# Performance work log

Measured on AMD Instinct MI355X. Metric: run time of the kernel, lower is better.

Reference implementation:

```python
import jax, jax.numpy as jnp
import numpy as np
import math

B, S, D, H, HD, R, F = 2, 2048, 1024, 16, 64, 32, 4096
EPS = 1e-5

def _layernorm(x, g, b):
    mu = jnp.mean(x, axis=-1, keepdims=True)
    var = jnp.mean(jnp.square(x - mu), axis=-1, keepdims=True)
    return (x - mu) * jax.lax.rsqrt(var + EPS) * g + b

def _gelu(x):
    # faithful tanh-approximation from the module
    c = math.sqrt(2.0 / math.pi)
    return 0.5 * x * (1.0 + jnp.tanh(c * (x + 0.044715 * x ** 3)))

def setup_inputs() -> dict:
    key = jax.random.key(0)
    ks = jax.random.split(key, 8)
    s = 0.02
    return dict(
        x=jax.random.normal(ks[0], (B, S, D), jnp.float32),
        ln1_g=jnp.ones((D,), jnp.float32), ln1_b=jnp.zeros((D,), jnp.float32),
        Wq=jax.random.normal(ks[1], (H, D, HD), jnp.float32) * s,
        bq=jnp.zeros((H, HD), jnp.float32),
        Wk=jax.random.normal(ks[2], (H, D, HD), jnp.float32) * s,
        bk=jnp.zeros((H, HD), jnp.float32),
        Wvd=jax.random.normal(ks[3], (H, D, R), jnp.float32) * s,
        bvd=jnp.zeros((H, R), jnp.float32),
        Wvu=jax.random.normal(ks[4], (H, R, HD), jnp.float32) * s,
        bvu=jnp.zeros((H, HD), jnp.float32),
        ln2_g=jnp.ones((D,), jnp.float32), ln2_b=jnp.zeros((D,), jnp.float32),
        W1=jax.random.normal(ks[5], (D, F), jnp.float32) * s,
        b1=jnp.zeros((F,), jnp.float32),
        W2=jax.random.normal(ks[6], (F, D), jnp.float32) * s,
        b2=jnp.zeros((D,), jnp.float32),
    )

def reference(x, ln1_g, ln1_b, Wq, bq, Wk, bk, Wvd, bvd, Wvu, bvu,
              ln2_g, ln2_b, W1, b1, W2, b2):
    Bx, Sx, Dx = x.shape
    y = x
    h = _layernorm(x, ln1_g, ln1_b)
    # all heads batched: [B,H,S,HD]
    q = jnp.einsum('bsd,hde->bhse', h, Wq) + bq[None, :, None, :]
    k = jnp.einsum('bsd,hde->bhse', h, Wk) + bk[None, :, None, :]
    vd = jnp.einsum('bsd,hdr->bhsr', h, Wvd) + bvd[None, :, None, :]
    v = jnp.einsum('bhsr,hre->bhse', vd, Wvu) + bvu[None, :, None, :]
    scores = jnp.einsum('bhse,bhte->bhst', q, k) / math.sqrt(Dx)  # NB: scaled by embed dim, as in source
    i = jnp.arange(Sx)
    mask = i[None, :] < i[:, None]  # key index < query index is masked (reversed causal, faithful)
    scores = jnp.where(mask[None, None, :, :], -jnp.inf, scores)
    attn = jax.nn.softmax(scores, axis=-1)
    o = jnp.einsum('bhst,bhte->bhse', attn, v)
    o = o.transpose(0, 2, 1, 3).reshape(Bx, Sx, Dx)  # concat heads
    x = o + y
    y = x
    h = _layernorm(x, ln2_g, ln2_b)
    h = _gelu(h @ W1 + b1)
    h = h @ W2 + b2
    return h + y
```

## Files before the change

kernel.cpp:

```cpp
#include <hip/hip_runtime.h>


typedef unsigned short u16;
typedef __attribute__((ext_vector_type(4))) float f32x4;
typedef __attribute__((ext_vector_type(8))) __bf16 bf16x8;

#define B_ 2
#define S_ 2048
#define D_ 1024
#define H_ 16
#define HD_ 64
#define R_ 32
#define F_ 4096
#define M_ (B_ * S_)
#define NQKV 2560
#define C2F 0.04508422002778011f

__device__ __forceinline__ u16 f2bf(float f) {
  union { float f; unsigned u; } v; v.f = f;
  unsigned u = v.u;
  return (u16)((u + 0x7FFFu + ((u >> 16) & 1u)) >> 16);
}
__device__ __forceinline__ float bf2f(u16 h) {
  union { unsigned u; float f; } v; v.u = ((unsigned)h) << 16;
  return v.f;
}
__device__ __forceinline__ unsigned pk_bf16(float lo, float hi) {
  unsigned r;
  asm volatile("v_cvt_pk_bf16_f32 %0, %1, %2" : "=v"(r) : "v"(lo), "v"(hi));
  return r;
}

typedef __attribute__((address_space(1))) void gvoid;
typedef __attribute__((address_space(3))) void lvoid;
__device__ __forceinline__ void gload_lds16(const void* g, void* l) {
  __builtin_amdgcn_global_load_lds((gvoid*)(void*)g, (lvoid*)l, 16, 0, 0);
}

__device__ __forceinline__ float gelu_f(float x) {
  float t = tanhf(0.7978845608028654f * (x + 0.044715f * x * x * x));
  return 0.5f * x * (1.0f + t);
}

__global__ __launch_bounds__(256) void wtrans(const float* __restrict__ in,
                                              u16* __restrict__ out,
                                              int Rr, int Cc, long ibs, long obs,
                                              float scale) {
  __shared__ float tile[32][33];
  const float* ip = in + (size_t)blockIdx.z * ibs;
  u16* op = out + (size_t)blockIdx.z * obs;
  int c0 = blockIdx.x * 32, r0 = blockIdx.y * 32;
  int tx = threadIdx.x & 31, ty = threadIdx.x >> 5;
#pragma unroll
  for (int j = 0; j < 32; j += 8)
    tile[ty + j][tx] = ip[(size_t)(r0 + ty + j) * Cc + c0 + tx];
  __syncthreads();
#pragma unroll
  for (int j = 0; j < 32; j += 8)
    op[(size_t)(c0 + ty + j) * Rr + r0 + tx] = f2bf(tile[tx][ty + j] * scale);
}

__global__ __launch_bounds__(256) void wconv(const float* __restrict__ in,
                                             u16* __restrict__ out, int n) {
  int i = (blockIdx.x * 256 + threadIdx.x) * 4;
  if (i < n) {
    float4 v = *(const float4*)&in[i];
    ushort4 o;
    o.x = f2bf(v.x); o.y = f2bf(v.y); o.z = f2bf(v.z); o.w = f2bf(v.w);
    *(ushort4*)&out[i] = o;
  }
}

__global__ __launch_bounds__(256) void bconcat(const float* __restrict__ bq,
                                               const float* __restrict__ bk,
                                               const float* __restrict__ bvd,
                                               float* __restrict__ o) {
  int i = blockIdx.x * 256 + threadIdx.x;
  if (i < NQKV) {
    float v = (i < 1024) ? bq[i] * C2F : (i < 2048 ? bk[i - 1024] : bvd[i - 2048]);
    o[i] = v;
  }
}

__global__ __launch_bounds__(256) void ln_kernel(const float* __restrict__ xin,
                                                 const float* __restrict__ addin,
                                                 const float* __restrict__ gam,
                                                 const float* __restrict__ bet,
                                                 u16* __restrict__ hout,
                                                 float* __restrict__ x2out) {
  int row = blockIdx.x, tid = threadIdx.x;
  size_t base = (size_t)row * D_ + tid * 4;
  float4 v = *(const float4*)&xin[base];
  if (addin) {
    float4 a = *(const float4*)&addin[base];
    v.x += a.x; v.y += a.y; v.z += a.z; v.w += a.w;
  }
  if (x2out) *(float4*)&x2out[base] = v;
  float s = v.x + v.y + v.z + v.w;
  float ss = v.x * v.x + v.y * v.y + v.z * v.z + v.w * v.w;
#pragma unroll
  for (int off = 32; off > 0; off >>= 1) {
    s += __shfl_down(s, off);
    ss += __shfl_down(ss, off);
  }
  __shared__ float red[8];
  int wv = tid >> 6;
  if ((tid & 63) == 0) { red[wv] = s; red[4 + wv] = ss; }
  __syncthreads();
  if (tid == 0) {
    float s1 = red[0] + red[1] + red[2] + red[3];
    float s2 = red[4] + red[5] + red[6] + red[7];
    float mu = s1 * (1.0f / D_);
    red[0] = mu;
    red[1] = s2 * (1.0f / D_) - mu * mu;
  }
  __syncthreads();
  float mu = red[0];
  float rstd = rsqrtf(red[1] + 1e-5f);
  int ci = tid * 4;
  ushort4 o;
  o.x = f2bf((v.x - mu) * rstd * gam[ci + 0] + bet[ci + 0]);
  o.y = f2bf((v.y - mu) * rstd * gam[ci + 1] + bet[ci + 1]);
  o.z = f2bf((v.z - mu) * rstd * gam[ci + 2] + bet[ci + 2]);
  o.w = f2bf((v.w - mu) * rstd * gam[ci + 3] + bet[ci + 3]);
  *(ushort4*)&hout[base] = o;
}

template <int MODE>
__global__ __launch_bounds__(256) void gemm_nt(const u16* __restrict__ A,
                                               const u16* __restrict__ Bt,
                                               int K, int lda, int ldb,
                                               const float* __restrict__ bias,
                                               const float* __restrict__ res,
                                               void* __restrict__ Cout,
                                               void* __restrict__ Cout2, int ldc) {
  __shared__ __align__(16) u16 As0[128 * 32];
  __shared__ __align__(16) u16 Bs0[128 * 32];
  __shared__ __align__(16) u16 As1[128 * 32];
  __shared__ __align__(16) u16 Bs1[128 * 32];
  int tid = threadIdx.x;
  int lane = tid & 63, wid = tid >> 6;
  int wm = wid >> 1, wn = wid & 1;
  int row0 = blockIdx.y * 128, col0 = blockIdx.x * 128;
  int l15 = lane & 15, g = lane >> 4;
  int srow = lane >> 2, scol = (lane & 3) * 8;
  f32x4 acc[4][4] = {};
  const u16* Ap = A + (size_t)row0 * lda;
  const u16* Bp = Bt + (size_t)col0 * ldb;

  auto STAGE = [&](u16* AS, u16* BS, int kk) {
#pragma unroll
    for (int i = 0; i < 2; ++i) {
      int c = wid * 2 + i;
      gload_lds16(Ap + (size_t)(c * 16 + srow) * lda + kk + scol, &AS[c * 512]);
      gload_lds16(Bp + (size_t)(c * 16 + srow) * ldb + kk + scol, &BS[c * 512]);
    }
  };
  auto COMPUTE = [&](const u16* AS, const u16* BS) {
    bf16x8 af[4], bfr[4];
#pragma unroll
    for (int t = 0; t < 4; ++t) {
      af[t] = *(const bf16x8*)&AS[(wm * 64 + t * 16 + l15) * 32 + g * 8];
      bfr[t] = *(const bf16x8*)&BS[(wn * 64 + t * 16 + l15) * 32 + g * 8];
    }
#pragma unroll
    for (int mt = 0; mt < 4; ++mt)
#pragma unroll
      for (int nt = 0; nt < 4; ++nt)
        acc[mt][nt] = __builtin_amdgcn_mfma_f32_16x16x32_bf16(af[mt], bfr[nt],
                                                              acc[mt][nt], 0, 0, 0);
  };

  STAGE(As0, Bs0, 0);
  __syncthreads();
  for (int k0 = 0; k0 < K; k0 += 64) {
    if (k0 + 32 < K) STAGE(As1, Bs1, k0 + 32);
    COMPUTE(As0, Bs0);
    __syncthreads();
    if (k0 + 64 < K) STAGE(As0, Bs0, k0 + 64);
    COMPUTE(As1, Bs1);
    __syncthreads();
  }

#pragma unroll
  for (int mt = 0; mt < 4; ++mt) {
#pragma unroll
    for (int nt = 0; nt < 4; ++nt) {
      int cc = col0 + wn * 64 + nt * 16 + l15;
      float bv = bias ? bias[cc] : 0.0f;
#pragma unroll
      for (int j = 0; j < 4; ++j) {
        int rr = row0 + wm * 64 + mt * 16 + g * 4 + j;
        float v = acc[mt][nt][j] + bv;
        if (MODE == 1) v = gelu_f(v);
        if (MODE == 2) {
          ((float*)Cout)[(size_t)rr * ldc + cc] = v + res[(size_t)rr * ldc + cc];
        } else {
          ((u16*)Cout)[(size_t)rr * ldc + cc] = f2bf(v);
        }
      }
    }
  }
  (void)Cout2;
}

template <int MODE>
__global__ __launch_bounds__(512, 2) void gemm8(
    const u16* __restrict__ A, const u16* __restrict__ Bt,
    int lda, int ldb, int nk,
    const float* __restrict__ bias,
    float* __restrict__ Cf, u16* __restrict__ Cb,
    u16* __restrict__ P1, u16* __restrict__ P2, u16* __restrict__ P3,
    int ldc) {
  extern __shared__ __align__(16) char smem[];
  int tid = threadIdx.x;
  int lane = tid & 63, wid = tid >> 6;
  int wm = wid >> 2, wn = wid & 3;
  int l15 = lane & 15, g = lane >> 4;
  int row0 = blockIdx.y * 256, col0 = blockIdx.x * 256;
  int koff = blockIdx.z * (nk * 64);
  const u16* Ap = A + (size_t)row0 * lda + koff;
  const u16* Bp = Bt + (size_t)col0 * ldb + koff;
  int trow = tid >> 3;
  int sbyte = ((tid & 7) * 16) ^ ((trow & 7) << 4);
  int xr = (l15 & 7) << 4;

  f32x4 acc[8][4] = {};

  auto STAGE_A = [&](int buf, int kt) {
#pragma unroll
    for (int l = 0; l < 4; ++l)
      gload_lds16((const char*)(Ap + (size_t)(l * 64 + trow) * lda + kt) + sbyte,
                  smem + buf * 65536 + (l * 64 + wid * 8) * 128);
  };
  auto STAGE_B = [&](int buf, int kt) {
#pragma unroll
    for (int l = 0; l < 4; ++l)
      gload_lds16((const char*)(Bp + (size_t)(l * 64 + trow) * ldb + kt) + sbyte,
                  smem + buf * 65536 + 32768 + (l * 64 + wid * 8) * 128);
  };

  STAGE_A(0, 0);
  STAGE_B(0, 0);
  asm volatile("s_waitcnt vmcnt(0)" ::: "memory");
  __builtin_amdgcn_sched_barrier(0);
  __builtin_amdgcn_s_barrier();

  int cur = 0;
  for (int it = 0; it < nk; ++it) {
    const char* Ab = smem + cur * 65536 + (wm * 128 + l15) * 128;
    const char* Bb = smem + cur * 65536 + 32768 + (wn * 64 + l15) * 128;
    bool nxt = (it + 1 < nk);
#pragma unroll
    for (int kk = 0; kk < 2; ++kk) {
      int kq = (kk * 64 + g * 16) ^ xr;
      bf16x8 bfr[4], af[8];
#pragma unroll
      for (int nt = 0; nt < 4; ++nt)
        bfr[nt] = *(const bf16x8*)(Bb + nt * 2048 + kq);
#pragma unroll
      for (int mt = 0; mt < 8; ++mt)
        af[mt] = *(const bf16x8*)(Ab + mt * 2048 + kq);
      if (nxt) {
        if (kk == 0) STAGE_A(cur ^ 1, (it + 1) * 64);
        else         STAGE_B(cur ^ 1, (it + 1) * 64);
      }
      __builtin_amdgcn_s_setprio(1);
#pragma unroll
      for (int mt = 0; mt < 8; ++mt)
#pragma unroll
        for (int nt = 0; nt < 4; ++nt)
          acc[mt][nt] = __builtin_amdgcn_mfma_f32_16x16x32_bf16(af[mt], bfr[nt],
                                                                acc[mt][nt], 0, 0, 0);
      __builtin_amdgcn_s_setprio(0);
    }
    asm volatile("s_waitcnt vmcnt(0)" ::: "memory");
    __builtin_amdgcn_sched_barrier(0);
    __builtin_amdgcn_s_barrier();
    cur ^= 1;
  }

  u16* pp = (u16*)nullptr;
  if (MODE == 4 && blockIdx.z != 0)
    pp = (blockIdx.z == 1) ? P1 : (blockIdx.z == 2 ? P2 : P3);
#pragma unroll
  for (int mt = 0; mt < 8; ++mt) {
#pragma unroll
    for (int nt = 0; nt < 4; ++nt) {
      int cc = col0 + wn * 64 + nt * 16 + l15;
      float bv = (MODE == 1) ? bias[cc] : 0.0f;
#pragma unroll
      for (int j = 0; j < 4; ++j) {
        int rr = row0 + wm * 128 + mt * 16 + g * 4 + j;
        float v = acc[mt][nt][j] + bv;
        if (MODE == 1) {
          Cb[(size_t)rr * ldc + cc] = f2bf(gelu_f(v));
        } else {
          if (blockIdx.z == 0) Cf[(size_t)rr * ldc + cc] = v;
          else                 pp[(size_t)rr * ldc + cc] = f2bf(v);
        }
      }
    }
  }
}

__global__ __launch_bounds__(256) void reduce2(float* __restrict__ out,
                                               const u16* __restrict__ p1,
                                               const u16* __restrict__ p2,
                                               const u16* __restrict__ p3,
                                               const float* __restrict__ b2,
                                               const float* __restrict__ x2) {
  int i = (blockIdx.x * 256 + threadIdx.x) * 4;
  float4 o = *(float4*)&out[i];
  ushort4 a = *(const ushort4*)&p1[i];
  ushort4 b = *(const ushort4*)&p2[i];
  ushort4 c = *(const ushort4*)&p3[i];
  float4 r = *(const float4*)&x2[i];
  int cix = i & (D_ - 1);
  o.x += bf2f(a.x) + bf2f(b.x) + bf2f(c.x) + b2[cix + 0] + r.x;
  o.y += bf2f(a.y) + bf2f(b.y) + bf2f(c.y) + b2[cix + 1] + r.y;
  o.z += bf2f(a.z) + bf2f(b.z) + bf2f(c.z) + b2[cix + 2] + r.z;
  o.w += bf2f(a.w) + bf2f(b.w) + bf2f(c.w) + b2[cix + 3] + r.w;
  *(float4*)&out[i] = o;
}

__global__ __launch_bounds__(256) void vu_kernel(const u16* __restrict__ vd,
                                                 const u16* __restrict__ wvu,
                                                 const float* __restrict__ bvu,
                                                 u16* __restrict__ v_t) {
  int t0 = blockIdx.x * 64, h = blockIdx.y, b = blockIdx.z;
  __shared__ u16 vds[64][32];
  __shared__ u16 vt[64][65];
  int tid = threadIdx.x;
  {
    int rr2 = tid >> 2, c8 = (tid & 3) * 8;
    *(bf16x8*)&vds[rr2][c8] =
        *(const bf16x8*)&vd[(size_t)(b * S_ + t0 + rr2) * NQKV + 2048 + h * R_ + c8];
  }
  __syncthreads();
  int e = tid & 63, tg = (tid >> 6) * 16;
  float wcol[32];
#pragma unroll
  for (int r = 0; r < 32; ++r) wcol[r] = bf2f(wvu[((size_t)h * R_ + r) * HD_ + e]);
  float bb = bvu[h * HD_ + e];
  for (int i = 0; i < 16; ++i) {
    int t = tg + i;
    float acc = bb;
#pragma unroll
    for (int r = 0; r < 32; ++r) acc += bf2f(vds[t][r]) * wcol[r];
    vt[t][e] = f2bf(acc);
  }
  __syncthreads();
  for (int idx = tid; idx < 64 * 64; idx += 256) {
    int e2 = idx >> 6, t2 = idx & 63;
    v_t[((size_t)(b * H_ + h) * HD_ + e2) * S_ + t0 + t2] = vt[t2][e2];
  }
}

__global__ __launch_bounds__(256) void attn_kernel(const u16* __restrict__ cqkv,
                                                   const u16* __restrict__ v_t,
                                                   float* __restrict__ o) {
  int tid = threadIdx.x;
  int lane = tid & 63, w = tid >> 6;
  int h = blockIdx.y, b = blockIdx.z;
  int r = lane & 15, g = lane >> 4;
  const u16* qp = cqkv + (size_t)(b * S_) * NQKV + h * HD_;
  const u16* kp = cqkv + (size_t)(b * S_) * NQKV + 1024 + h * HD_;
  const u16* vp = v_t + (size_t)(b * H_ + h) * HD_ * S_;

  __shared__ u16 Ks[2][64 * 64];
  __shared__ u16 Vs[2][64 * 64];
  __shared__ u16 Pl[4][16 * 64];
  u16* Pw = Pl[w];

  int srow = w * 16 + (lane >> 3);
  int ssw = ((lane & 7) * 16) ^ (((lane >> 3) & 7) << 4);

  int xr = (r & 7) << 4;
  int kq0 = ((g * 16) ^ xr) >> 1;
  int kq1 = ((64 + g * 16) ^ xr) >> 1;

  auto STAGE = [&](int buf, int kt) {
    gload_lds16((const char*)(kp + (size_t)(kt + srow) * NQKV) + ssw,
                &Ks[buf][w * 1024]);
    gload_lds16((const char*)(kp + (size_t)(kt + srow + 8) * NQKV) + ssw,
                &Ks[buf][w * 1024 + 512]);
    gload_lds16((const char*)(vp + (size_t)srow * S_ + kt) + ssw,
                &Vs[buf][w * 1024]);
    gload_lds16((const char*)(vp + (size_t)(srow + 8) * S_ + kt) + ssw,
                &Vs[buf][w * 1024 + 512]);
  };

#pragma unroll 1
  for (int half = 0; half < 2; ++half) {
    int qb = half ? (S_ - 64) - blockIdx.x * 64 : blockIdx.x * 64;
    int s0 = qb + w * 16;
    int qrow = s0 + r;

    bf16x8 aq0 = *(const bf16x8*)(qp + (size_t)(s0 + r) * NQKV + g * 8);
    bf16x8 aq1 = *(const bf16x8*)(qp + (size_t)(s0 + r) * NQKV + 32 + g * 8);

    f32x4 oa[4] = {};
    float m_ = -1e30f, l_ = 0.0f;

    STAGE(0, qb);
    __syncthreads();
    int cur = 0;
    for (int kt = qb; kt < S_; kt += 64) {
      if (kt + 64 < S_) STAGE(cur ^ 1, kt + 64);
      const u16* Kb = &Ks[cur][0];
      const u16* Vb = &Vs[cur][0];

      f32x4 sc[4] = {};
#pragma unroll
      for (int blk = 0; blk < 4; ++blk) {
        bf16x8 a0 = *(const bf16x8*)&Kb[((blk * 16 + r) << 6) + kq0];
        bf16x8 a1 = *(const bf16x8*)&Kb[((blk * 16 + r) << 6) + kq1];
        sc[blk] = __builtin_amdgcn_mfma_f32_16x16x32_bf16(a0, aq0, sc[blk], 0, 0, 0);
        sc[blk] = __builtin_amdgcn_mfma_f32_16x16x32_bf16(a1, aq1, sc[blk], 0, 0, 0);
      }

      float p[16];
      if (kt == qb) {
#pragma unroll
        for (int blk = 0; blk < 4; ++blk)
#pragma unroll
          for (int j = 0; j < 4; ++j) {
            int kk = kt + blk * 16 + g * 4 + j;
            p[blk * 4 + j] = (kk < qrow) ? -1e30f : sc[blk][j];
          }
      } else {
#pragma unroll
        for (int blk = 0; blk < 4; ++blk)
#pragma unroll
          for (int j = 0; j < 4; ++j) p[blk * 4 + j] = sc[blk][j];
      }
      float mx = p[0];
#pragma unroll
      for (int i = 1; i < 16; ++i) mx = fmaxf(mx, p[i]);
      mx = fmaxf(mx, __shfl_xor(mx, 16));
      mx = fmaxf(mx, __shfl_xor(mx, 32));
      float mn = fmaxf(m_, mx);
      float scl = __builtin_amdgcn_exp2f(m_ - mn);
      m_ = mn;
      float sm = 0.0f;
#pragma unroll
      for (int i = 0; i < 16; ++i) {
        p[i] = __builtin_amdgcn_exp2f(p[i] - mn);
        sm += p[i];
      }
      sm += __shfl_xor(sm, 16);
      sm += __shfl_xor(sm, 32);
      l_ = l_ * scl + sm;
#pragma unroll
      for (int et = 0; et < 4; ++et) oa[et] *= scl;

#pragma unroll
      for (int blk = 0; blk < 4; ++blk) {
        uint2 pk;
        pk.x = pk_bf16(p[blk * 4 + 0], p[blk * 4 + 1]);
        pk.y = pk_bf16(p[blk * 4 + 2], p[blk * 4 + 3]);
        *(uint2*)&Pw[(r << 6) + ((((blk << 5) + (g << 3)) ^ xr) >> 1)] = pk;
      }
      asm volatile("s_waitcnt lgkmcnt(0)" ::: "memory");
      bf16x8 pb0 = *(const bf16x8*)&Pw[(r << 6) + kq0];
      bf16x8 pb1 = *(const bf16x8*)&Pw[(r << 6) + kq1];
#pragma unroll
      for (int et = 0; et < 4; ++et) {
        bf16x8 v0 = *(const bf16x8*)&Vb[((et * 16 + r) << 6) + kq0];
        bf16x8 v1 = *(const bf16x8*)&Vb[((et * 16 + r) << 6) + kq1];
        oa[et] = __builtin_amdgcn_mfma_f32_16x16x32_bf16(v0, pb0, oa[et], 0, 0, 0);
        oa[et] = __builtin_amdgcn_mfma_f32_16x16x32_bf16(v1, pb1, oa[et], 0, 0, 0);
      }
      __syncthreads();
      cur ^= 1;
    }

    float inv = 1.0f / l_;
#pragma unroll
    for (int et = 0; et < 4; ++et)
#pragma unroll
      for (int j = 0; j < 4; ++j)
        o[(size_t)(b * S_ + s0 + r) * D_ + h * HD_ + et * 16 + g * 4 + j] =
            oa[et][j] * inv;
  }
}

namespace {
struct GemmAttrInit {
  GemmAttrInit() {
    hipFuncSetAttribute((const void*)gemm8<1>,
                        hipFuncAttributeMaxDynamicSharedMemorySize, 131072);
    hipFuncSetAttribute((const void*)gemm8<4>,
                        hipFuncAttributeMaxDynamicSharedMemorySize, 131072);
  }
};
GemmAttrInit _gemm_attr_init;
}

extern "C" void kernel_launch(void* const* d_in, const int* in_sizes, int n_in,
                              void* d_out, int out_size, void* d_ws, size_t ws_size,
                              hipStream_t stream) {
  const float* x = (const float*)d_in[0];
  const float* ln1_g = (const float*)d_in[1];
  const float* ln1_b = (const float*)d_in[2];
  const float* Wq = (const float*)d_in[3];
  const float* bq = (const float*)d_in[4];
  const float* Wk = (const float*)d_in[5];
  const float* bk = (const float*)d_in[6];
  const float* Wvd = (const float*)d_in[7];
  const float* bvd = (const float*)d_in[8];
  const float* Wvu = (const float*)d_in[9];
  const float* bvu = (const float*)d_in[10];
  const float* ln2_g = (const float*)d_in[11];
  const float* ln2_b = (const float*)d_in[12];
  const float* W1 = (const float*)d_in[13];
  const float* b1 = (const float*)d_in[14];
  const float* W2 = (const float*)d_in[15];
  const float* b2 = (const float*)d_in[16];
  float* out = (float*)d_out;
  (void)in_sizes; (void)n_in; (void)out_size; (void)ws_size;

  char* ws = (char*)d_ws;
  const size_t MB = 1024 * 1024;
  const size_t KB = 1024;
  u16* wqkvT = (u16*)(ws + 0);
  u16* wvuB = (u16*)(ws + 5 * MB);
  float* bqkv = (float*)(ws + 5 * MB + 64 * KB);
  u16* w1T = (u16*)(ws + 5 * MB + 384 * KB);
  u16* w2T = (u16*)(ws + 13 * MB + 384 * KB);
  u16* hbuf = (u16*)(ws + 21 * MB + 384 * KB);
  u16* cqkv = (u16*)(ws + 29 * MB + 384 * KB);
  u16* vT = (u16*)(ws + 49 * MB + 384 * KB);
  float* ob = (float*)(ws + 57 * MB + 384 * KB);
  float* x2 = (float*)(ws + 73 * MB + 384 * KB);
  u16* ubuf = cqkv;
  u16* p1 = (u16*)(ws + 0);
  u16* p2 = (u16*)hbuf;
  u16* p3 = (u16*)vT;

  dim3 blk(256);
  wtrans<<<dim3(2, 32, 16), blk, 0, stream>>>(Wq, wqkvT, 1024, 64, 65536L, 65536L, C2F);
  wtrans<<<dim3(2, 32, 16), blk, 0, stream>>>(Wk, wqkvT + 1024 * 1024, 1024, 64,
                                              65536L, 65536L, 1.0f);
  wtrans<<<dim3(1, 32, 16), blk, 0, stream>>>(Wvd, wqkvT + 2048 * 1024, 1024, 32,
                                              32768L, 32768L, 1.0f);
  wconv<<<dim3(32), blk, 0, stream>>>(Wvu, wvuB, H_ * R_ * HD_);
  bconcat<<<dim3(10), blk, 0, stream>>>(bq, bk, bvd, bqkv);
  wtrans<<<dim3(128, 32, 1), blk, 0, stream>>>(W1, w1T, 1024, 4096, 0L, 0L, 1.0f);
  wtrans<<<dim3(32, 128, 1), blk, 0, stream>>>(W2, w2T, 4096, 1024, 0L, 0L, 1.0f);
  ln_kernel<<<dim3(M_), blk, 0, stream>>>(x, (const float*)nullptr, ln1_g, ln1_b,
                                          hbuf, (float*)nullptr);
  gemm_nt<0><<<dim3(20, 32), blk, 0, stream>>>(hbuf, wqkvT, 1024, 1024, 1024, bqkv,
                                               (const float*)nullptr, (void*)cqkv,
                                               (void*)nullptr, NQKV);
  vu_kernel<<<dim3(S_ / 64, H_, B_), blk, 0, stream>>>(cqkv, wvuB, bvu, vT);
  attn_kernel<<<dim3(S_ / 128, H_, B_), blk, 0, stream>>>(cqkv, vT, ob);
  ln_kernel<<<dim3(M_), blk, 0, stream>>>(x, ob, ln2_g, ln2_b, hbuf, x2);
  gemm8<1><<<dim3(16, 16, 1), dim3(512), 131072, stream>>>(
      hbuf, w1T, 1024, 1024, 16, b1, (float*)nullptr, ubuf,
      (u16*)nullptr, (u16*)nullptr, (u16*)nullptr, 4096);
  gemm8<4><<<dim3(4, 16, 4), dim3(512), 131072, stream>>>(
      ubuf, w2T, 4096, 4096, 16, (const float*)nullptr, out, (u16*)nullptr,
      p1, p2, p3, 1024);
  reduce2<<<dim3(M_ * D_ / 1024), blk, 0, stream>>>(out, p1, p2, p3, b2, x2);
}
```

Measured before the change: 241.6 us.

## Restructure attention kernel: 512 threads, 128-query tiles, triple-buffered K/V pipeline

The attention kernel now uses 8 waves per block, with each block covering 128 queries per half instead of 64, so every K/V tile staged into LDS is shared by twice as many query rows. K/V staging goes through a three-deep dynamic-shared-memory ring with explicit vmcnt waits and one barrier per iteration, replacing the double buffer that synced at the end of each step. Q is now loaded through LDS, and waves whose queries lie entirely past a key tile skip its compute. The grid is reordered so heads and batch are the fastest-varying dimensions. The cost is more shared memory per block and some waves idling at the diagonal tile.

```diff
diff --git a/kernel.cpp b/kernel.cpp
--- a/kernel.cpp
+++ b/kernel.cpp
@@ -357,23 +357,22 @@
   }
 }
 
-__global__ __launch_bounds__(256) void attn_kernel(const u16* __restrict__ cqkv,
-                                                   const u16* __restrict__ v_t,
-                                                   float* __restrict__ o) {
+__global__ __launch_bounds__(512, 2) void attn_kernel(const u16* __restrict__ cqkv,
+                                                      const u16* __restrict__ v_t,
+                                                      float* __restrict__ o) {
+  extern __shared__ __align__(16) u16 kv[];
+  __shared__ u16 Pl[8][16 * 64];
   int tid = threadIdx.x;
   int lane = tid & 63, w = tid >> 6;
-  int h = blockIdx.y, b = blockIdx.z;
+  int h = blockIdx.x, b = blockIdx.y;
+  int bx = blockIdx.z;
   int r = lane & 15, g = lane >> 4;
   const u16* qp = cqkv + (size_t)(b * S_) * NQKV + h * HD_;
   const u16* kp = cqkv + (size_t)(b * S_) * NQKV + 1024 + h * HD_;
   const u16* vp = v_t + (size_t)(b * H_ + h) * HD_ * S_;
-
-  __shared__ u16 Ks[2][64 * 64];
-  __shared__ u16 Vs[2][64 * 64];
-  __shared__ u16 Pl[4][16 * 64];
   u16* Pw = Pl[w];
 
-  int srow = w * 16 + (lane >> 3);
+  int srow = w * 8 + (lane >> 3);
   int ssw = ((lane & 7) * 16) ^ (((lane >> 3) & 7) << 4);
 
   int xr = (r & 7) << 4;
@@ -381,99 +380,115 @@
   int kq1 = ((64 + g * 16) ^ xr) >> 1;
 
   auto STAGE = [&](int buf, int kt) {
+    u16* base = kv + buf * 8192;
     gload_lds16((const char*)(kp + (size_t)(kt + srow) * NQKV) + ssw,
-                &Ks[buf][w * 1024]);
-    gload_lds16((const char*)(kp + (size_t)(kt + srow + 8) * NQKV) + ssw,
-                &Ks[buf][w * 1024 + 512]);
+                base + w * 512);
     gload_lds16((const char*)(vp + (size_t)srow * S_ + kt) + ssw,
-                &Vs[buf][w * 1024]);
-    gload_lds16((const char*)(vp + (size_t)(srow + 8) * S_ + kt) + ssw,
-                &Vs[buf][w * 1024 + 512]);
+                base + 4096 + w * 512);
   };
 
 #pragma unroll 1
   for (int half = 0; half < 2; ++half) {
-    int qb = half ? (S_ - 64) - blockIdx.x * 64 : blockIdx.x * 64;
+    int qb = half ? (S_ - 128) - bx * 128 : bx * 128;
     int s0 = qb + w * 16;
     int qrow = s0 + r;
 
-    bf16x8 aq0 = *(const bf16x8*)(qp + (size_t)(s0 + r) * NQKV + g * 8);
-    bf16x8 aq1 = *(const bf16x8*)(qp + (size_t)(s0 + r) * NQKV + 32 + g * 8);
+    gload_lds16((const char*)(qp + (size_t)(s0 + (lane >> 3)) * NQKV) + ssw, Pw);
+    gload_lds16((const char*)(qp + (size_t)(s0 + 8 + (lane >> 3)) * NQKV) + ssw,
+                Pw + 512);
+    asm volatile("s_waitcnt vmcnt(0)" ::: "memory");
+    __builtin_amdgcn_sched_barrier(0);
+    __builtin_amdgcn_s_barrier();
+    __builtin_amdgcn_sched_barrier(0);
+    bf16x8 aq0 = *(const bf16x8*)&Pw[(r << 6) + kq0];
+    bf16x8 aq1 = *(const bf16x8*)&Pw[(r << 6) + kq1];
 
     f32x4 oa[4] = {};
     float m_ = -1e30f, l_ = 0.0f;
 
+    int nt = (S_ - qb) >> 6;
     STAGE(0, qb);
-    __syncthreads();
-    int cur = 0;
-    for (int kt = qb; kt < S_; kt += 64) {
-      if (kt + 64 < S_) STAGE(cur ^ 1, kt + 64);
-      const u16* Kb = &Ks[cur][0];
-      const u16* Vb = &Vs[cur][0];
-
-      f32x4 sc[4] = {};
-#pragma unroll
-      for (int blk = 0; blk < 4; ++blk) {
-        bf16x8 a0 = *(const bf16x8*)&Kb[((blk * 16 + r) << 6) + kq0];
-        bf16x8 a1 = *(const bf16x8*)&Kb[((blk * 16 + r) << 6) + kq1];
-        sc[blk] = __builtin_amdgcn_mfma_f32_16x16x32_bf16(a0, aq0, sc[blk], 0, 0, 0);
-        sc[blk] = __builtin_amdgcn_mfma_f32_16x16x32_bf16(a1, aq1, sc[blk], 0, 0, 0);
+    STAGE(1, qb + 64);
+
+    for (int it = 0; it < nt; ++it) {
+      int kt = qb + it * 64;
+      if (it + 1 < nt) {
+        asm volatile("s_waitcnt vmcnt(2)" ::: "memory");
+      } else {
+        asm volatile("s_waitcnt vmcnt(0)" ::: "memory");
       }
-
-      float p[16];
-      if (kt == qb) {
-#pragma unroll
-        for (int blk = 0; blk < 4; ++blk)
-#pragma unroll
-          for (int j = 0; j < 4; ++j) {
-            int kk = kt + blk * 16 + g * 4 + j;
-            p[blk * 4 + j] = (kk < qrow) ? -1e30f : sc[blk][j];
-          }
-      } else {
-#pragma unroll
-        for (int blk = 0; blk < 4; ++blk)
-#pragma unroll
-          for (int j = 0; j < 4; ++j) p[blk * 4 + j] = sc[blk][j];
+      __builtin_amdgcn_sched_barrier(0);
+      __builtin_amdgcn_s_barrier();
+      __builtin_amdgcn_sched_barrier(0);
+      if (it + 2 < nt) STAGE((it + 2) % 3, qb + (it + 2) * 64);
+
+      if (kt + 64 > s0) {
+        const u16* Kb = kv + (it % 3) * 8192;
+        const u16* Vb = Kb + 4096;
+
+        f32x4 sc[4] = {};
+#pragma unroll
+        for (int blk = 0; blk < 4; ++blk) {
+          bf16x8 a0 = *(const bf16x8*)&Kb[((blk * 16 + r) << 6) + kq0];
+          bf16x8 a1 = *(const bf16x8*)&Kb[((blk * 16 + r) << 6) + kq1];
+          sc[blk] = __builtin_amdgcn_mfma_f32_16x16x32_bf16(a0, aq0, sc[blk], 0, 0, 0);
+          sc[blk] = __builtin_amdgcn_mfma_f32_16x16x32_bf16(a1, aq1, sc[blk], 0, 0, 0);
+        }
+
+        float p[16];
+        if ((qrow & ~63) == kt) {
+#pragma unroll
+          for (int blk = 0; blk < 4; ++blk)
+#pragma unroll
+            for (int j = 0; j < 4; ++j) {
+              int kk = kt + blk * 16 + g * 4 + j;
+              p[blk * 4 + j] = (kk < qrow) ? -1e30f : sc[blk][j];
+            }
+        } else {
+#pragma unroll
+          for (int blk = 0; blk < 4; ++blk)
+#pragma unroll
+            for (int j = 0; j < 4; ++j) p[blk * 4 + j] = sc[blk][j];
+        }
+        float mx = p[0];
+#pragma unroll
+        for (int i = 1; i < 16; ++i) mx = fmaxf(mx, p[i]);
+        mx = fmaxf(mx, __shfl_xor(mx, 16));
+        mx = fmaxf(mx, __shfl_xor(mx, 32));
+        float mn = fmaxf(m_, mx);
+        float scl = __builtin_amdgcn_exp2f(m_ - mn);
+        m_ = mn;
+        float sm = 0.0f;
+#pragma unroll
+        for (int i = 0; i < 16; ++i) {
+          p[i] = __builtin_amdgcn_exp2f(p[i] - mn);
+          sm += p[i];
+        }
+        sm += __shfl_xor(sm, 16);
+        sm += __shfl_xor(sm, 32);
+        l_ = l_ * scl + sm;
+#pragma unroll
+        for (int et = 0; et < 4; ++et) oa[et] *= scl;
+
+#pragma unroll
+        for (int blk = 0; blk < 4; ++blk) {
+          uint2 pk;
+          pk.x = pk_bf16(p[blk * 4 + 0], p[blk * 4 + 1]);
+          pk.y = pk_bf16(p[blk * 4 + 2], p[blk * 4 + 3]);
+          *(uint2*)&Pw[(r << 6) + ((((blk << 5) + (g << 3)) ^ xr) >> 1)] = pk;
+        }
+        asm volatile("s_waitcnt lgkmcnt(0)" ::: "memory");
+        __builtin_amdgcn_sched_barrier(0);
+        bf16x8 pb0 = *(const bf16x8*)&Pw[(r << 6) + kq0];
+        bf16x8 pb1 = *(const bf16x8*)&Pw[(r << 6) + kq1];
+#pragma unroll
+        for (int et = 0; et < 4; ++et) {
+          bf16x8 v0 = *(const bf16x8*)&Vb[((et * 16 + r) << 6) + kq0];
+          bf16x8 v1 = *(const bf16x8*)&Vb[((et * 16 + r) << 6) + kq1];
+          oa[et] = __builtin_amdgcn_mfma_f32_16x16x32_bf16(v0, pb0, oa[et], 0, 0, 0);
+          oa[et] = __builtin_amdgcn_mfma_f32_16x16x32_bf16(v1, pb1, oa[et], 0, 0, 0);
+        }
       }
-      float mx = p[0];
-#pragma unroll
-      for (int i = 1; i < 16; ++i) mx = fmaxf(mx, p[i]);
-      mx = fmaxf(mx, __shfl_xor(mx, 16));
-      mx = fmaxf(mx, __shfl_xor(mx, 32));
-      float mn = fmaxf(m_, mx);
-      float scl = __builtin_amdgcn_exp2f(m_ - mn);
-      m_ = mn;
-      float sm = 0.0f;
-#pragma unroll
-      for (int i = 0; i < 16; ++i) {
-        p[i] = __builtin_amdgcn_exp2f(p[i] - mn);
-        sm += p[i];
-      }
-      sm += __shfl_xor(sm, 16);
-      sm += __shfl_xor(sm, 32);
-      l_ = l_ * scl + sm;
-#pragma unroll
-      for (int et = 0; et < 4; ++et) oa[et] *= scl;
-
-#pragma unroll
-      for (int blk = 0; blk < 4; ++blk) {
-        uint2 pk;
-        pk.x = pk_bf16(p[blk * 4 + 0], p[blk * 4 + 1]);
-        pk.y = pk_bf16(p[blk * 4 + 2], p[blk * 4 + 3]);
-        *(uint2*)&Pw[(r << 6) + ((((blk << 5) + (g << 3)) ^ xr) >> 1)] = pk;
-      }
-      asm volatile("s_waitcnt lgkmcnt(0)" ::: "memory");
-      bf16x8 pb0 = *(const bf16x8*)&Pw[(r << 6) + kq0];
-      bf16x8 pb1 = *(const bf16x8*)&Pw[(r << 6) + kq1];
-#pragma unroll
-      for (int et = 0; et < 4; ++et) {
-        bf16x8 v0 = *(const bf16x8*)&Vb[((et * 16 + r) << 6) + kq0];
-        bf16x8 v1 = *(const bf16x8*)&Vb[((et * 16 + r) << 6) + kq1];
-        oa[et] = __builtin_amdgcn_mfma_f32_16x16x32_bf16(v0, pb0, oa[et], 0, 0, 0);
-        oa[et] = __builtin_amdgcn_mfma_f32_16x16x32_bf16(v1, pb1, oa[et], 0, 0, 0);
-      }
-      __syncthreads();
-      cur ^= 1;
     }
 
     float inv = 1.0f / l_;
@@ -493,6 +508,8 @@
                         hipFuncAttributeMaxDynamicSharedMemorySize, 131072);
     hipFuncSetAttribute((const void*)gemm8<4>,
                         hipFuncAttributeMaxDynamicSharedMemorySize, 131072);
+    hipFuncSetAttribute((const void*)attn_kernel,
+                        hipFuncAttributeMaxDynamicSharedMemorySize, 49152);
   }
 };
 GemmAttrInit _gemm_attr_init;
@@ -555,7 +572,7 @@
                                                (const float*)nullptr, (void*)cqkv,
                                                (void*)nullptr, NQKV);
   vu_kernel<<<dim3(S_ / 64, H_, B_), blk, 0, stream>>>(cqkv, wvuB, bvu, vT);
-  attn_kernel<<<dim3(S_ / 128, H_, B_), blk, 0, stream>>>(cqkv, vT, ob);
+  attn_kernel<<<dim3(H_, B_, 8), dim3(512), 49152, stream>>>(cqkv, vT, ob);
   ln_kernel<<<dim3(M_), blk, 0, stream>>>(x, ob, ln2_g, ln2_b, hbuf, x2);
   gemm8<1><<<dim3(16, 16, 1), dim3(512), 131072, stream>>>(
       hbuf, w1T, 1024, 1024, 16, b1, (float*)nullptr, ubuf,
```

After: 232.4 us. 1.04x faster.
